# Kernel optimization log

Measured on AMD Instinct MI355X. Metric: run time of the kernel, lower is better.

Reference implementation:

```python
import jax, jax.numpy as jnp
import numpy as np

TEMPERATURE = 2.0
RAD2DEG = 180.0 / np.pi


def _safe_norm(diff, axis=-1):
    # L2 norm with zero (sub)gradient at 0, matching torch's convention and
    # avoiding NaNs on the (later-discarded) diagonal of pairwise distances.
    d2 = jnp.sum(diff * diff, axis=axis)
    pos = d2 > 0
    return jnp.where(pos, jnp.sqrt(jnp.where(pos, d2, 1.0)), 0.0)


def _rot6d_to_matrix(d6):
    # pytorch3d.transforms.rotation_6d_to_matrix: Gram-Schmidt on two 3-vectors.
    a1, a2 = d6[..., :3], d6[..., 3:6]
    b1 = a1 / jnp.linalg.norm(a1, axis=-1, keepdims=True)
    a2p = a2 - jnp.sum(b1 * a2, axis=-1, keepdims=True) * b1
    b2 = a2p / jnp.linalg.norm(a2p, axis=-1, keepdims=True)
    b3 = jnp.cross(b1, b2)
    return jnp.stack([b1, b2, b3], axis=-2)  # [n, 3, 3], rows b1,b2,b3


def _pose_error(pose):
    rot = _rot6d_to_matrix(pose[:, :6])                    # [n,3,3]
    div = jnp.power(jnp.linalg.det(rot), 1.0 / 3.0)[:, None, None]
    rot = rot / div
    t = pose[:, 6:]                                        # [n,3]
    # trace(rot_i @ rot_j^T) = sum_ab rot_i[a,b]*rot_j[a,b]
    r_trace = jnp.einsum('iab,jab->ij', rot, rot)          # [n,n]
    cos_theta = (r_trace - 1.0) / 2.0
    theta = jnp.arccos(jnp.clip(cos_theta, -1.0, 1.0)) * RAD2DEG
    shift = _safe_norm(t[:, None, :] - t[None, :, :]) * 100.0
    return theta, shift


def reference(features, labels):
    n = features.shape[0]
    theta_diffs, shift_diffs = _pose_error(labels)

    # FeatureSimilarity('l2'): -||f_i - f_j|| / t
    logits = -_safe_norm(features[:, None, :] - features[None, :, :]) / TEMPERATURE
    logits = logits - jax.lax.stop_gradient(jnp.max(logits, axis=1, keepdims=True))
    exp_logits = jnp.exp(logits)

    # Drop diagonal -> [n, n-1], preserving ascending column order (masked_select).
    cols = jnp.arange(n - 1)
    jidx = cols[None, :] + (cols[None, :] >= jnp.arange(n)[:, None]).astype(cols.dtype)
    take = lambda x: jnp.take_along_axis(x, jidx, axis=1)
    L = take(logits)          # [n, n-1]
    E = take(exp_logits)      # [n, n-1]
    TD = take(theta_diffs)    # [n, n-1]
    SD = take(shift_diffs)    # [n, n-1]

    # Vectorize the k-loop: M[i,k,j] = diffs[i,j] >= diffs[i,k]
    mt = TD[:, None, :] >= TD[:, :, None]                 # [n, n-1, n-1]
    ms = SD[:, None, :] >= SD[:, :, None]
    denom_t = jnp.sum(jnp.where(mt, E[:, None, :], 0.0), axis=-1)  # [n, n-1]
    denom_s = jnp.sum(jnp.where(ms, E[:, None, :], 0.0), axis=-1)

    pos_log_probs = (2.0 * L - jnp.log(denom_t) - jnp.log(denom_s)) / 2.0
    return -jnp.sum(pos_log_probs) / (n * (n - 1))


def setup_inputs() -> dict:
    key = jax.random.key(0)
    k1, k2 = jax.random.split(key)
    features = jax.random.normal(k1, (512, 256), dtype=jnp.float32)
    labels = jax.random.normal(k2, (512, 9), dtype=jnp.float32)
    return {"features": features, "labels": labels}
```

## Files before the change

kernel.cpp:

```cpp
#include <hip/hip_runtime.h>
#include <math.h>

#define N 512
#define D 256
#define ITILE 2
#define NPAIRS 261632.0f

typedef unsigned long long u64;
#define SW(x) ((x) ^ (((x) >> 4) & 15))

__constant__ float kRad2Deg = 57.29577951308232f;

__global__ __launch_bounds__(64) void prep_kernel(
        const float* __restrict__ f,
        const float* __restrict__ labels,
        float* __restrict__ rot,
        float* __restrict__ tvec,
        float* __restrict__ nrm,
        float* __restrict__ acc) {
    const int i = blockIdx.x;
    const int l = threadIdx.x;

    const float4 v = ((const float4*)(f + i * D))[l];
    float ss = v.x * v.x + v.y * v.y + v.z * v.z + v.w * v.w;
#pragma unroll
    for (int off = 32; off > 0; off >>= 1) ss += __shfl_down(ss, off, 64);

    if (l == 0) {
        nrm[i] = ss;
        const float* p = labels + i * 9;
        float a1x = p[0], a1y = p[1], a1z = p[2];
        float a2x = p[3], a2y = p[4], a2z = p[5];
        float n1 = sqrtf(a1x * a1x + a1y * a1y + a1z * a1z);
        float b1x = a1x / n1, b1y = a1y / n1, b1z = a1z / n1;
        float dp = b1x * a2x + b1y * a2y + b1z * a2z;
        float cx = a2x - dp * b1x, cy = a2y - dp * b1y, cz = a2z - dp * b1z;
        float n2 = sqrtf(cx * cx + cy * cy + cz * cz);
        float b2x = cx / n2, b2y = cy / n2, b2z = cz / n2;
        float b3x = b1y * b2z - b1z * b2y;
        float b3y = b1z * b2x - b1x * b2z;
        float b3z = b1x * b2y - b1y * b2x;
        float det = b1x * (b2y * b3z - b2z * b3y)
                  - b1y * (b2x * b3z - b2z * b3x)
                  + b1z * (b2x * b3y - b2y * b3x);
        float inv = 1.0f / cbrtf(det);
        float* r = rot + i * 9;
        r[0] = b1x * inv; r[1] = b1y * inv; r[2] = b1z * inv;
        r[3] = b2x * inv; r[4] = b2y * inv; r[5] = b2z * inv;
        r[6] = b3x * inv; r[7] = b3y * inv; r[8] = b3z * inv;
        tvec[i * 3 + 0] = p[6];
        tvec[i * 3 + 1] = p[7];
        tvec[i * 3 + 2] = p[8];
        if (i == 0) acc[0] = 0.0f;
    }
}

__global__ __launch_bounds__(512) void rowdata_kernel(
        const float* __restrict__ f,
        const float* __restrict__ rot,
        const float* __restrict__ tvec,
        const float* __restrict__ nrm,
        float* __restrict__ E,
        float* __restrict__ TD,
        float* __restrict__ SD,
        float* __restrict__ acc) {
    __shared__ __attribute__((aligned(16))) float lds_fi[ITILE * D];
    __shared__ float red[8];

    const int j  = threadIdx.x;
    const int i0 = blockIdx.x * ITILE;

    lds_fi[j] = f[i0 * D + j];
    __syncthreads();

    float dot0 = 0.0f, dot1 = 0.0f;
    const float4* __restrict__ fj4 = (const float4*)(f + j * D);
#pragma unroll 16
    for (int kk = 0; kk < D / 4; ++kk) {
        const float4 v = fj4[kk];
        const float4 a = *(const float4*)&lds_fi[kk * 4];
        const float4 b = *(const float4*)&lds_fi[D + kk * 4];
        dot0 += a.x * v.x; dot0 += a.y * v.y; dot0 += a.z * v.z; dot0 += a.w * v.w;
        dot1 += b.x * v.x; dot1 += b.y * v.y; dot1 += b.z * v.z; dot1 += b.w * v.w;
    }
    const float nj  = nrm[j];
    const float dotr[2] = { dot0, dot1 };

    float rj[9];
#pragma unroll
    for (int c = 0; c < 9; ++c) rj[c] = rot[j * 9 + c];
    const float tjx = tvec[j * 3 + 0];
    const float tjy = tvec[j * 3 + 1];
    const float tjz = tvec[j * 3 + 2];

    float lsum = 0.0f;
#pragma unroll
    for (int r = 0; r < ITILE; ++r) {
        const int i = i0 + r;
        float tr = 0.0f;
#pragma unroll
        for (int c = 0; c < 9; ++c) tr += rot[i * 9 + c] * rj[c];
        float ct = (tr - 1.0f) * 0.5f;
        ct = fminf(1.0f, fmaxf(-1.0f, ct));
        float theta = acosf(ct) * kRad2Deg;

        float dx = tvec[i * 3 + 0] - tjx;
        float dy = tvec[i * 3 + 1] - tjy;
        float dz = tvec[i * 3 + 2] - tjz;
        float sd2 = dx * dx + dy * dy + dz * dz;
        float shift = (sd2 > 0.0f ? sqrtf(sd2) : 0.0f) * 100.0f;

        float d2 = nrm[i] + nj - 2.0f * dotr[r];
        float L, Ev;
        if (j == i) { L = 0.0f; Ev = 0.0f; }
        else {
            float dist = (d2 > 0.0f ? sqrtf(d2) : 0.0f);
            L  = -dist * 0.5f;
            Ev = expf(L);
        }
        E[i * N + j]  = Ev;
        TD[i * N + j] = theta;
        SD[i * N + j] = shift;
        lsum += L;
    }

#pragma unroll
    for (int off = 32; off > 0; off >>= 1) lsum += __shfl_down(lsum, off, 64);
    const int lane = j & 63, wid = j >> 6;
    if (lane == 0) red[wid] = lsum;
    __syncthreads();
    if (j == 0) {
        float s = 0.0f;
#pragma unroll
        for (int w = 0; w < 8; ++w) s += red[w];
        atomicAdd(acc, s);
    }
}

__global__ __launch_bounds__(256) void sortdenom_kernel(
        const float* __restrict__ E,
        const float* __restrict__ TD,
        const float* __restrict__ SD,
        float* __restrict__ acc) {
    __shared__ u64   qT[512], qS[512];
    __shared__ float sT[512], sS[512];
    __shared__ int   lT[512], lS[512];
    __shared__ float redA[4], redB[4];
    __shared__ float diag_part_sh;

    const int t = threadIdx.x;
    const int i = blockIdx.x;
    const float* __restrict__ er = E  + i * N;
    const float* __restrict__ tr = TD + i * N;
    const float* __restrict__ sr = SD + i * N;

    const float e0 = er[t], e1 = er[t + 256];
    const float t0 = tr[t], t1 = tr[t + 256];
    const float s0 = sr[t], s1 = sr[t + 256];
    const float dT = tr[i], dS = sr[i];

    float dtd = ((t0 >= dT) ? e0 : 0.0f) + ((t1 >= dT) ? e1 : 0.0f);
    float dsd = ((s0 >= dS) ? e0 : 0.0f) + ((s1 >= dS) ? e1 : 0.0f);
#pragma unroll
    for (int off = 32; off > 0; off >>= 1) {
        dtd += __shfl_down(dtd, off, 64);
        dsd += __shfl_down(dsd, off, 64);
    }
    const int lane = t & 63, wid = t >> 6;
    if (lane == 0) { redA[wid] = dtd; redB[wid] = dsd; }

    qT[SW(t)]       = ((u64)__float_as_uint(t0) << 32) | (u64)__float_as_uint(e0);
    qT[SW(t + 256)] = ((u64)__float_as_uint(t1) << 32) | (u64)__float_as_uint(e1);
    qS[SW(t)]       = ((u64)__float_as_uint(s0) << 32) | (u64)__float_as_uint(e0);
    qS[SW(t + 256)] = ((u64)__float_as_uint(s1) << 32) | (u64)__float_as_uint(e1);
    __syncthreads();

    if (t == 0) {
        float a = redA[0] + redA[1] + redA[2] + redA[3];
        float b = redB[0] + redB[1] + redB[2] + redB[3];
        diag_part_sh = 0.5f * (logf(a) + logf(b));
    }

    for (unsigned k = 2; k <= 512; k <<= 1) {
        for (unsigned jj = k >> 1; jj >= 1; jj >>= 1) {
            __syncthreads();
            const unsigned a = ((t & ~(jj - 1)) << 1) | (t & (jj - 1));
            const unsigned b = a | jj;
            const bool up = ((a & k) == 0);
            {
                u64 va = qT[SW(a)], vb = qT[SW(b)];
                if (up ? (va > vb) : (va < vb)) { qT[SW(a)] = vb; qT[SW(b)] = va; }
            }
            {
                u64 va = qS[SW(a)], vb = qS[SW(b)];
                if (up ? (va > vb) : (va < vb)) { qS[SW(a)] = vb; qS[SW(b)] = va; }
            }
        }
    }
    __syncthreads();

    {
        const u64 v0 = qT[SW(t)],       v1 = qT[SW(t + 256)];
        sT[t]       = __uint_as_float((unsigned)v0);
        sT[t + 256] = __uint_as_float((unsigned)v1);
        const unsigned h0 = (unsigned)(v0 >> 32), h1 = (unsigned)(v1 >> 32);
        const unsigned hp1 = (unsigned)(qT[SW(t + 255)] >> 32);
        lT[t]       = (t == 0 || (unsigned)(qT[SW(t - 1)] >> 32) != h0) ? t : 0;
        lT[t + 256] = (hp1 != h1) ? (t + 256) : 0;
    }
    {
        const u64 v0 = qS[SW(t)],       v1 = qS[SW(t + 256)];
        sS[t]       = __uint_as_float((unsigned)v0);
        sS[t + 256] = __uint_as_float((unsigned)v1);
        const unsigned h0 = (unsigned)(v0 >> 32), h1 = (unsigned)(v1 >> 32);
        const unsigned hp1 = (unsigned)(qS[SW(t + 255)] >> 32);
        lS[t]       = (t == 0 || (unsigned)(qS[SW(t - 1)] >> 32) != h0) ? t : 0;
        lS[t + 256] = (hp1 != h1) ? (t + 256) : 0;
    }
    __syncthreads();

    for (int st = 1; st < 512; st <<= 1) {
        float a0 = (t + st < 512) ? sT[t + st] : 0.0f;
        float a1 = (t + 256 + st < 512) ? sT[t + 256 + st] : 0.0f;
        float b0 = (t + st < 512) ? sS[t + st] : 0.0f;
        float b1 = (t + 256 + st < 512) ? sS[t + 256 + st] : 0.0f;
        int   m0 = (t >= st) ? lT[t - st] : 0;
        int   m1 = lT[t + 256 - st];
        int   n0 = (t >= st) ? lS[t - st] : 0;
        int   n1 = lS[t + 256 - st];
        __syncthreads();
        sT[t] += a0; sT[t + 256] += a1;
        sS[t] += b0; sS[t + 256] += b1;
        lT[t] = max(lT[t], m0); lT[t + 256] = max(lT[t + 256], m1);
        lS[t] = max(lS[t], n0); lS[t + 256] = max(lS[t + 256], n1);
        __syncthreads();
    }

    float term = logf(sT[lT[t]]) + logf(sT[lT[t + 256]])
               + logf(sS[lS[t]]) + logf(sS[lS[t + 256]]);
#pragma unroll
    for (int off = 32; off > 0; off >>= 1) term += __shfl_down(term, off, 64);
    __syncthreads();
    if (lane == 0) redA[wid] = term;
    __syncthreads();
    if (t == 0) {
        float tt = redA[0] + redA[1] + redA[2] + redA[3];
        atomicAdd(acc, -0.5f * tt + diag_part_sh);
    }
}

__global__ void finalize_kernel(const float* __restrict__ acc,
                                float* __restrict__ out) {
    out[0] = -acc[0] / NPAIRS;
}

extern "C" void kernel_launch(void* const* d_in, const int* in_sizes, int n_in,
                              void* d_out, int out_size, void* d_ws, size_t ws_size,
                              hipStream_t stream) {
    const float* f      = (const float*)d_in[0];
    const float* labels = (const float*)d_in[1];
    float* out = (float*)d_out;
    float* ws  = (float*)d_ws;

    float* rot  = ws;
    float* tvec = rot + N * 9;
    float* nrm  = tvec + N * 3;
    float* acc  = nrm + N;
    float* E    = acc + 4;
    float* TD   = E + N * N;
    float* SD   = TD + N * N;

    prep_kernel<<<N, 64, 0, stream>>>(f, labels, rot, tvec, nrm, acc);
    rowdata_kernel<<<N / ITILE, 512, 0, stream>>>(f, rot, tvec, nrm, E, TD, SD, acc);
    sortdenom_kernel<<<N, 256, 0, stream>>>(E, TD, SD, acc);
    finalize_kernel<<<1, 1, 0, stream>>>(acc, out);
}
```

Before: 57.36 us.

## Fuse row-data and sort kernels, drop global E/TD/SD buffers and finalize launch

Merges the pairwise-distance/pose kernel and the bitonic sort/scan kernel into one kernel per row with 512 threads. One thread computes each column's values straight into LDS, so the three N×N global intermediate arrays are gone. Half the threads now sort the theta keys and half the shift keys in parallel. The finalize kernel is replaced by a last-block-done atomic counter. In exchange, each block now recomputes a full row of dot products with one row per block, which doubles feature re-reads compared with the previous two-rows-per-block tiling.

```diff
diff --git a/kernel.cpp b/kernel.cpp
--- a/kernel.cpp
+++ b/kernel.cpp
@@ -3,7 +3,6 @@
 
 #define N 512
 #define D 256
-#define ITILE 2
 #define NPAIRS 261632.0f
 
 typedef unsigned long long u64;
@@ -17,7 +16,8 @@
         float* __restrict__ rot,
         float* __restrict__ tvec,
         float* __restrict__ nrm,
-        float* __restrict__ acc) {
+        float* __restrict__ acc,
+        unsigned* __restrict__ cnt) {
     const int i = blockIdx.x;
     const int l = threadIdx.x;
 
@@ -51,147 +51,94 @@
         tvec[i * 3 + 0] = p[6];
         tvec[i * 3 + 1] = p[7];
         tvec[i * 3 + 2] = p[8];
-        if (i == 0) acc[0] = 0.0f;
+        if (i == 0) { acc[0] = 0.0f; cnt[0] = 0u; }
     }
 }
 
-__global__ __launch_bounds__(512) void rowdata_kernel(
+__global__ __launch_bounds__(512) void fused_row_kernel(
         const float* __restrict__ f,
         const float* __restrict__ rot,
         const float* __restrict__ tvec,
         const float* __restrict__ nrm,
-        float* __restrict__ E,
-        float* __restrict__ TD,
-        float* __restrict__ SD,
-        float* __restrict__ acc) {
-    __shared__ __attribute__((aligned(16))) float lds_fi[ITILE * D];
-    __shared__ float red[8];
-
-    const int j  = threadIdx.x;
-    const int i0 = blockIdx.x * ITILE;
-
-    lds_fi[j] = f[i0 * D + j];
-    __syncthreads();
-
-    float dot0 = 0.0f, dot1 = 0.0f;
-    const float4* __restrict__ fj4 = (const float4*)(f + j * D);
-#pragma unroll 16
-    for (int kk = 0; kk < D / 4; ++kk) {
-        const float4 v = fj4[kk];
-        const float4 a = *(const float4*)&lds_fi[kk * 4];
-        const float4 b = *(const float4*)&lds_fi[D + kk * 4];
-        dot0 += a.x * v.x; dot0 += a.y * v.y; dot0 += a.z * v.z; dot0 += a.w * v.w;
-        dot1 += b.x * v.x; dot1 += b.y * v.y; dot1 += b.z * v.z; dot1 += b.w * v.w;
-    }
-    const float nj  = nrm[j];
-    const float dotr[2] = { dot0, dot1 };
-
-    float rj[9];
-#pragma unroll
-    for (int c = 0; c < 9; ++c) rj[c] = rot[j * 9 + c];
-    const float tjx = tvec[j * 3 + 0];
-    const float tjy = tvec[j * 3 + 1];
-    const float tjz = tvec[j * 3 + 2];
-
-    float lsum = 0.0f;
-#pragma unroll
-    for (int r = 0; r < ITILE; ++r) {
-        const int i = i0 + r;
-        float tr = 0.0f;
-#pragma unroll
-        for (int c = 0; c < 9; ++c) tr += rot[i * 9 + c] * rj[c];
-        float ct = (tr - 1.0f) * 0.5f;
-        ct = fminf(1.0f, fmaxf(-1.0f, ct));
-        float theta = acosf(ct) * kRad2Deg;
-
-        float dx = tvec[i * 3 + 0] - tjx;
-        float dy = tvec[i * 3 + 1] - tjy;
-        float dz = tvec[i * 3 + 2] - tjz;
-        float sd2 = dx * dx + dy * dy + dz * dz;
-        float shift = (sd2 > 0.0f ? sqrtf(sd2) : 0.0f) * 100.0f;
-
-        float d2 = nrm[i] + nj - 2.0f * dotr[r];
-        float L, Ev;
-        if (j == i) { L = 0.0f; Ev = 0.0f; }
-        else {
-            float dist = (d2 > 0.0f ? sqrtf(d2) : 0.0f);
-            L  = -dist * 0.5f;
-            Ev = expf(L);
-        }
-        E[i * N + j]  = Ev;
-        TD[i * N + j] = theta;
-        SD[i * N + j] = shift;
-        lsum += L;
-    }
-
-#pragma unroll
-    for (int off = 32; off > 0; off >>= 1) lsum += __shfl_down(lsum, off, 64);
-    const int lane = j & 63, wid = j >> 6;
-    if (lane == 0) red[wid] = lsum;
-    __syncthreads();
-    if (j == 0) {
-        float s = 0.0f;
-#pragma unroll
-        for (int w = 0; w < 8; ++w) s += red[w];
-        atomicAdd(acc, s);
-    }
-}
-
-__global__ __launch_bounds__(256) void sortdenom_kernel(
-        const float* __restrict__ E,
-        const float* __restrict__ TD,
-        const float* __restrict__ SD,
-        float* __restrict__ acc) {
+        float* __restrict__ acc,
+        unsigned* __restrict__ cnt,
+        float* __restrict__ out) {
+    __shared__ __attribute__((aligned(16))) float4 lds_fi[D / 4];
     __shared__ u64   qT[512], qS[512];
     __shared__ float sT[512], sS[512];
     __shared__ int   lT[512], lS[512];
-    __shared__ float redA[4], redB[4];
-    __shared__ float diag_part_sh;
-
-    const int t = threadIdx.x;
-    const int i = blockIdx.x;
-    const float* __restrict__ er = E  + i * N;
-    const float* __restrict__ tr = TD + i * N;
-    const float* __restrict__ sr = SD + i * N;
-
-    const float e0 = er[t], e1 = er[t + 256];
-    const float t0 = tr[t], t1 = tr[t + 256];
-    const float s0 = sr[t], s1 = sr[t + 256];
-    const float dT = tr[i], dS = sr[i];
-
-    float dtd = ((t0 >= dT) ? e0 : 0.0f) + ((t1 >= dT) ? e1 : 0.0f);
-    float dsd = ((s0 >= dS) ? e0 : 0.0f) + ((s1 >= dS) ? e1 : 0.0f);
+    __shared__ float redA[8], redB[8], redC[8];
+    __shared__ float sh_dT, sh_dS;
+
+    const int t  = threadIdx.x;
+    const int i  = blockIdx.x;
+    const int tp = t & 255;
+    const int lane = t & 63, wid = t >> 6;
+
+    if (t < D / 4) lds_fi[t] = ((const float4*)(f + i * D))[t];
+    __syncthreads();
+
+    float dot = 0.0f;
+    const float4* __restrict__ fj4 = (const float4*)(f + t * D);
+#pragma unroll 8
+    for (int kk = 0; kk < D / 4; ++kk) {
+        const float4 v = fj4[kk];
+        const float4 a = lds_fi[kk];
+        dot += a.x * v.x; dot += a.y * v.y; dot += a.z * v.z; dot += a.w * v.w;
+    }
+
+    float rj[9];
+#pragma unroll
+    for (int c = 0; c < 9; ++c) rj[c] = rot[t * 9 + c];
+    float tr = 0.0f;
+#pragma unroll
+    for (int c = 0; c < 9; ++c) tr += rot[i * 9 + c] * rj[c];
+    float ct = (tr - 1.0f) * 0.5f;
+    ct = fminf(1.0f, fmaxf(-1.0f, ct));
+    const float theta = acosf(ct) * kRad2Deg;
+
+    const float dx = tvec[i * 3 + 0] - tvec[t * 3 + 0];
+    const float dy = tvec[i * 3 + 1] - tvec[t * 3 + 1];
+    const float dz = tvec[i * 3 + 2] - tvec[t * 3 + 2];
+    const float sd2 = dx * dx + dy * dy + dz * dz;
+    const float shift = (sd2 > 0.0f ? sqrtf(sd2) : 0.0f) * 100.0f;
+
+    const float d2 = nrm[i] + nrm[t] - 2.0f * dot;
+    float L, Ev;
+    if (t == i) { L = 0.0f; Ev = 0.0f; }
+    else {
+        const float dist = (d2 > 0.0f ? sqrtf(d2) : 0.0f);
+        L  = -dist * 0.5f;
+        Ev = expf(L);
+    }
+
+    if (t == i) { sh_dT = theta; sh_dS = shift; }
+    const u64 eb = (u64)__float_as_uint(Ev);
+    qT[SW(t)] = ((u64)__float_as_uint(theta) << 32) | eb;
+    qS[SW(t)] = ((u64)__float_as_uint(shift) << 32) | eb;
+    __syncthreads();
+
+    float dtd = (theta >= sh_dT) ? Ev : 0.0f;
+    float dsd = (shift >= sh_dS) ? Ev : 0.0f;
+    float lpart = L;
 #pragma unroll
     for (int off = 32; off > 0; off >>= 1) {
-        dtd += __shfl_down(dtd, off, 64);
-        dsd += __shfl_down(dsd, off, 64);
-    }
-    const int lane = t & 63, wid = t >> 6;
-    if (lane == 0) { redA[wid] = dtd; redB[wid] = dsd; }
-
-    qT[SW(t)]       = ((u64)__float_as_uint(t0) << 32) | (u64)__float_as_uint(e0);
-    qT[SW(t + 256)] = ((u64)__float_as_uint(t1) << 32) | (u64)__float_as_uint(e1);
-    qS[SW(t)]       = ((u64)__float_as_uint(s0) << 32) | (u64)__float_as_uint(e0);
-    qS[SW(t + 256)] = ((u64)__float_as_uint(s1) << 32) | (u64)__float_as_uint(e1);
-    __syncthreads();
-
-    if (t == 0) {
-        float a = redA[0] + redA[1] + redA[2] + redA[3];
-        float b = redB[0] + redB[1] + redB[2] + redB[3];
-        diag_part_sh = 0.5f * (logf(a) + logf(b));
-    }
+        dtd   += __shfl_down(dtd, off, 64);
+        dsd   += __shfl_down(dsd, off, 64);
+        lpart += __shfl_down(lpart, off, 64);
+    }
+    if (lane == 0) { redA[wid] = dtd; redB[wid] = dsd; redC[wid] = lpart; }
 
     for (unsigned k = 2; k <= 512; k <<= 1) {
         for (unsigned jj = k >> 1; jj >= 1; jj >>= 1) {
             __syncthreads();
-            const unsigned a = ((t & ~(jj - 1)) << 1) | (t & (jj - 1));
+            const unsigned a = ((tp & ~(jj - 1)) << 1) | (tp & (jj - 1));
             const unsigned b = a | jj;
             const bool up = ((a & k) == 0);
-            {
+            if (t < 256) {
                 u64 va = qT[SW(a)], vb = qT[SW(b)];
                 if (up ? (va > vb) : (va < vb)) { qT[SW(a)] = vb; qT[SW(b)] = va; }
-            }
-            {
+            } else {
                 u64 va = qS[SW(a)], vb = qS[SW(b)];
                 if (up ? (va > vb) : (va < vb)) { qS[SW(a)] = vb; qS[SW(b)] = va; }
             }
@@ -199,59 +146,76 @@
     }
     __syncthreads();
 
-    {
-        const u64 v0 = qT[SW(t)],       v1 = qT[SW(t + 256)];
-        sT[t]       = __uint_as_float((unsigned)v0);
-        sT[t + 256] = __uint_as_float((unsigned)v1);
+    float diag_part = 0.0f, lsum = 0.0f;
+    if (t == 0) {
+        float a = 0.0f, b = 0.0f;
+#pragma unroll
+        for (int w = 0; w < 8; ++w) { a += redA[w]; b += redB[w]; lsum += redC[w]; }
+        diag_part = 0.5f * (logf(a) + logf(b));
+    }
+
+    if (t < 256) {
+        const u64 v0 = qT[SW(tp)], v1 = qT[SW(tp + 256)];
+        sT[tp]       = __uint_as_float((unsigned)v0);
+        sT[tp + 256] = __uint_as_float((unsigned)v1);
         const unsigned h0 = (unsigned)(v0 >> 32), h1 = (unsigned)(v1 >> 32);
-        const unsigned hp1 = (unsigned)(qT[SW(t + 255)] >> 32);
-        lT[t]       = (t == 0 || (unsigned)(qT[SW(t - 1)] >> 32) != h0) ? t : 0;
-        lT[t + 256] = (hp1 != h1) ? (t + 256) : 0;
-    }
-    {
-        const u64 v0 = qS[SW(t)],       v1 = qS[SW(t + 256)];
-        sS[t]       = __uint_as_float((unsigned)v0);
-        sS[t + 256] = __uint_as_float((unsigned)v1);
+        const unsigned hp = (unsigned)(qT[SW(tp + 255)] >> 32);
+        lT[tp]       = (tp == 0 || (unsigned)(qT[SW(tp - 1)] >> 32) != h0) ? tp : 0;
+        lT[tp + 256] = (hp != h1) ? (tp + 256) : 0;
+    } else {
+        const u64 v0 = qS[SW(tp)], v1 = qS[SW(tp + 256)];
+        sS[tp]       = __uint_as_float((unsigned)v0);
+        sS[tp + 256] = __uint_as_float((unsigned)v1);
         const unsigned h0 = (unsigned)(v0 >> 32), h1 = (unsigned)(v1 >> 32);
-        const unsigned hp1 = (unsigned)(qS[SW(t + 255)] >> 32);
-        lS[t]       = (t == 0 || (unsigned)(qS[SW(t - 1)] >> 32) != h0) ? t : 0;
-        lS[t + 256] = (hp1 != h1) ? (t + 256) : 0;
+        const unsigned hp = (unsigned)(qS[SW(tp + 255)] >> 32);
+        lS[tp]       = (tp == 0 || (unsigned)(qS[SW(tp - 1)] >> 32) != h0) ? tp : 0;
+        lS[tp + 256] = (hp != h1) ? (tp + 256) : 0;
     }
     __syncthreads();
 
     for (int st = 1; st < 512; st <<= 1) {
-        float a0 = (t + st < 512) ? sT[t + st] : 0.0f;
-        float a1 = (t + 256 + st < 512) ? sT[t + 256 + st] : 0.0f;
-        float b0 = (t + st < 512) ? sS[t + st] : 0.0f;
-        float b1 = (t + 256 + st < 512) ? sS[t + 256 + st] : 0.0f;
-        int   m0 = (t >= st) ? lT[t - st] : 0;
-        int   m1 = lT[t + 256 - st];
-        int   n0 = (t >= st) ? lS[t - st] : 0;
-        int   n1 = lS[t + 256 - st];
+        float a0, a1; int m0, m1;
+        if (t < 256) {
+            a0 = (tp + st < 512) ? sT[tp + st] : 0.0f;
+            a1 = (tp + 256 + st < 512) ? sT[tp + 256 + st] : 0.0f;
+            m0 = (tp >= st) ? lT[tp - st] : 0;
+            m1 = lT[tp + 256 - st];
+        } else {
+            a0 = (tp + st < 512) ? sS[tp + st] : 0.0f;
+            a1 = (tp + 256 + st < 512) ? sS[tp + 256 + st] : 0.0f;
+            m0 = (tp >= st) ? lS[tp - st] : 0;
+            m1 = lS[tp + 256 - st];
+        }
         __syncthreads();
-        sT[t] += a0; sT[t + 256] += a1;
-        sS[t] += b0; sS[t + 256] += b1;
-        lT[t] = max(lT[t], m0); lT[t + 256] = max(lT[t + 256], m1);
-        lS[t] = max(lS[t], n0); lS[t + 256] = max(lS[t + 256], n1);
+        if (t < 256) {
+            sT[tp] += a0; sT[tp + 256] += a1;
+            lT[tp] = max(lT[tp], m0); lT[tp + 256] = max(lT[tp + 256], m1);
+        } else {
+            sS[tp] += a0; sS[tp + 256] += a1;
+            lS[tp] = max(lS[tp], m0); lS[tp + 256] = max(lS[tp + 256], m1);
+        }
         __syncthreads();
     }
 
-    float term = logf(sT[lT[t]]) + logf(sT[lT[t + 256]])
-               + logf(sS[lS[t]]) + logf(sS[lS[t + 256]]);
+    float term = logf(sT[lT[t]]) + logf(sS[lS[t]]);
 #pragma unroll
     for (int off = 32; off > 0; off >>= 1) term += __shfl_down(term, off, 64);
     __syncthreads();
     if (lane == 0) redA[wid] = term;
     __syncthreads();
+
     if (t == 0) {
-        float tt = redA[0] + redA[1] + redA[2] + redA[3];
-        atomicAdd(acc, -0.5f * tt + diag_part_sh);
-    }
-}
-
-__global__ void finalize_kernel(const float* __restrict__ acc,
-                                float* __restrict__ out) {
-    out[0] = -acc[0] / NPAIRS;
+        float tt = 0.0f;
+#pragma unroll
+        for (int w = 0; w < 8; ++w) tt += redA[w];
+        atomicAdd(acc, lsum - 0.5f * tt + diag_part);
+        __threadfence();
+        const unsigned old = atomicAdd(cnt, 1u);
+        if (old == (unsigned)(gridDim.x - 1)) {
+            const float total = atomicAdd(acc, 0.0f);
+            out[0] = -total / NPAIRS;
+        }
+    }
 }
 
 extern "C" void kernel_launch(void* const* d_in, const int* in_sizes, int n_in,
@@ -262,16 +226,12 @@
     float* out = (float*)d_out;
     float* ws  = (float*)d_ws;
 
-    float* rot  = ws;
-    float* tvec = rot + N * 9;
-    float* nrm  = tvec + N * 3;
-    float* acc  = nrm + N;
-    float* E    = acc + 4;
-    float* TD   = E + N * N;
-    float* SD   = TD + N * N;
-
-    prep_kernel<<<N, 64, 0, stream>>>(f, labels, rot, tvec, nrm, acc);
-    rowdata_kernel<<<N / ITILE, 512, 0, stream>>>(f, rot, tvec, nrm, E, TD, SD, acc);
-    sortdenom_kernel<<<N, 256, 0, stream>>>(E, TD, SD, acc);
-    finalize_kernel<<<1, 1, 0, stream>>>(acc, out);
+    float*    rot  = ws;
+    float*    tvec = rot + N * 9;
+    float*    nrm  = tvec + N * 3;
+    float*    acc  = nrm + N;
+    unsigned* cnt  = (unsigned*)(acc + 1);
+
+    prep_kernel<<<N, 64, 0, stream>>>(f, labels, rot, tvec, nrm, acc, cnt);
+    fused_row_kernel<<<N, 512, 0, stream>>>(f, rot, tvec, nrm, acc, cnt, out);
 }
```

After: 60.44 us. 5.4% more time.
